# Kernel tuning notes

Hardware: AMD Instinct MI355X
Metric: run time of the kernel (lower is better)

The kernel has to match this reference:

```python
import jax, jax.numpy as jnp
import numpy as np
import math
from math import factorial

EPS = 1e-8
N_ATOMS = 20000
K_NEI = 32
N_RBF = 12
RBF_GAMMA = 1.0
DIMS = [(3, 24), (24, 12), (12, 4)]
# (i, f, o) = (input angular order, filter order, output order), from Convolution.C
CG_PATHS = [(0,0,0),(0,1,1),(1,0,1),(1,1,0),(1,1,1),(1,1,2),(0,2,2),(1,2,1),(1,2,2),(2,2,0),(2,2,1),(2,2,2),(2,0,2),(2,1,1),(2,1,2)]


def _su2_cg(j1, m1, j2, m2, j3, m3):
    if m3 != m1 + m2:
        return 0.0
    f = factorial
    vmin = int(max(-j1 + j2 + m3, -j1 + m1, 0))
    vmax = int(min(j2 + j3 + m1, j3 - j1 + j2, j3 + m3))
    c = ((2 * j3 + 1) * f(j3 + j1 - j2) * f(j3 - j1 + j2) * f(j1 + j2 - j3)
         * f(j3 + m3) * f(j3 - m3)
         / (f(j1 + j2 + j3 + 1) * f(j1 - m1) * f(j1 + m1) * f(j2 - m2) * f(j2 + m2))) ** 0.5
    s = 0.0
    for v in range(vmin, vmax + 1):
        s += (-1) ** (v + j2 + m2) * f(j2 + j3 + m1 - v) * f(j1 - m1 + v) / (
            f(v) * f(j3 - j1 + j2 - v) * f(j3 + m3 - v) * f(j1 - j2 - m3 + v))
    return c * s


def _q(l):
    # change of basis real->complex spherical harmonics (e3nn convention)
    q = np.zeros((2 * l + 1, 2 * l + 1), dtype=complex)
    for m in range(-l, 0):
        q[l + m, l + abs(m)] = 1 / np.sqrt(2)
        q[l + m, l - abs(m)] = -1j / np.sqrt(2)
    q[l, l] = 1.0
    for m in range(1, l + 1):
        q[l + m, l + abs(m)] = (-1) ** m / np.sqrt(2)
        q[l + m, l - abs(m)] = 1j * (-1) ** m / np.sqrt(2)
    return (-1j) ** l * q


def _real_cg(i, f, o):
    C = np.zeros((2 * i + 1, 2 * f + 1, 2 * o + 1), dtype=complex)
    for a, m1 in enumerate(range(-i, i + 1)):
        for b, m2 in enumerate(range(-f, f + 1)):
            for c, m3 in enumerate(range(-o, o + 1)):
                C[a, b, c] = _su2_cg(i, m1, f, m2, o, m3)
    C = np.einsum('ij,kl,mn,ikn->jlm', _q(i), _q(f), np.conj(_q(o).T), C)
    return np.real(C).transpose(2, 0, 1).astype(np.float32)  # [2o+1, 2i+1, 2f+1]


CG = {(i, f, o): jnp.asarray(_real_cg(i, f, o)) for (i, f, o) in CG_PATHS}
RBF_MU = jnp.asarray(np.linspace(0.0, 8.0, N_RBF).astype(np.float32))


def _sh(vec):
    # real spherical harmonics as in class Y (l=1 is the raw vector, l=2 divided by r^2)
    x, y, z = vec[..., 0], vec[..., 1], vec[..., 2]
    r2 = jnp.maximum(x * x + y * y + z * z, EPS)
    y2 = jnp.stack([x * y / r2,
                    y * z / r2,
                    (-x * x - y * y + 2.0 * z * z) / (2.0 * math.sqrt(3.0) * r2),
                    z * x / r2,
                    (x * x - y * y) / (2.0 * r2)], axis=-1)
    return {0: jnp.ones(vec.shape[:-1] + (1,), vec.dtype), 1: vec, 2: y2}


def _ssp(x):  # eta: shifted softplus (SchNet-style scalar nonlinearity)
    return jax.nn.softplus(x) - math.log(2.0)


def _self_interaction(V, w, b):
    O = {k: jnp.einsum('ncm,dc->ndm', Vk, w) for k, Vk in V.items()}
    O[0] = O[0] + b[None, :, None]  # bias only on angular order 0
    return O


def _model(V, nei_idx, Ys, rbf, siA_w, siA_b, rw1, rb1, rw2, rb2, siB_w, siB_b, nl_b):
    V = _self_interaction(V, siA_w, siA_b)
    N, C = nei_idx.shape[0], rw2.shape[1]
    O = {l: jnp.zeros((N, C, 2 * l + 1), rbf.dtype) for l in range(3)}
    for p, (i, f, o) in enumerate(CG_PATHS):
        # per-path radial MLP: 12 -> 12 (relu) -> C
        h = jax.nn.relu(jnp.einsum('nkb,hb->nkh', rbf, rw1[p]) + rb1[p])
        r = jnp.einsum('nkh,ch->nkc', h, rw2[p]) + rb2[p]              # [N,K,C]
        Vg = V[i][nei_idx]                                              # [N,K,C,2i+1]
        cif = jnp.einsum('nkc,nkf,nkci->ncif', r, Ys[f], Vg)            # sum over neighbors
        O[o] = O[o] + jnp.einsum('oif,ncif->nco', CG[(i, f, o)], cif)
    # Norm: per-atom L2 norm over (channel, m)
    V = {k: Vk / jnp.sqrt(jnp.maximum(jnp.sum(Vk * Vk, axis=(1, 2), keepdims=True), EPS))
         for k, Vk in O.items()}
    V = _self_interaction(V, siB_w, siB_b)
    # NonLinearity (faithful to source: norm is taken over ALL atoms and m, per channel)
    out = {0: _ssp(V[0])}
    for k in (1, 2):
        temp = jnp.sqrt(jnp.einsum('acm,acm->c', V[k], V[k])) + nl_b[k - 1]
        out[k] = V[k] * temp[None, :, None]
    return out


def _forward(atom_types, nei_idx, nei_vec, layers, dense):
    N = atom_types.shape[0]
    dt = nei_vec.dtype
    V = {0: jax.nn.one_hot(atom_types, 3, dtype=dt)[:, :, None],
         1: jnp.zeros((N, 3, 3), dt),
         2: jnp.zeros((N, 3, 5), dt)}
    dist = jnp.sqrt(jnp.maximum(jnp.sum(nei_vec * nei_vec, axis=-1), EPS))   # [N,K]
    rbf = jnp.exp(-RBF_GAMMA * (dist[..., None] - RBF_MU) ** 2)              # [N,K,12]
    Ys = _sh(nei_vec)
    for lp in layers:
        V = _model(V, nei_idx, Ys, rbf, *lp)
    E = jnp.sum(V[0], axis=0)[:, 0]                                          # [4]
    dw1, db1, dw2, db2, dw3, db3 = dense
    E = jax.nn.elu(dw1 @ E + db1)
    E = dw2 @ E + db2
    E = dw3 @ E + db3
    return E  # [1]


def setup_inputs() -> dict:
    key = jax.random.key(0)
    ks = iter(jax.random.split(key, 64))
    inp = {}
    inp['atom_types'] = jax.random.randint(next(ks), (N_ATOMS,), 0, 3, dtype=jnp.int32)
    inp['nei_idx'] = jax.random.randint(next(ks), (N_ATOMS, K_NEI), 0, N_ATOMS, dtype=jnp.int32)
    inp['nei_vec'] = jax.random.normal(next(ks), (N_ATOMS, K_NEI, 3), jnp.float32) * 2.0
    for l, (din, dout) in enumerate(DIMS, start=1):
        inp[f'l{l}_siA_w'] = jax.random.normal(next(ks), (dout, din)) / np.sqrt(din)
        inp[f'l{l}_siA_b'] = jnp.zeros((dout,))
        inp[f'l{l}_rw1'] = jax.random.normal(next(ks), (15, N_RBF, N_RBF)) / np.sqrt(N_RBF)
        inp[f'l{l}_rb1'] = jnp.zeros((15, N_RBF))
        inp[f'l{l}_rw2'] = jax.random.normal(next(ks), (15, dout, N_RBF)) / np.sqrt(N_RBF)
        inp[f'l{l}_rb2'] = jnp.zeros((15, dout))
        inp[f'l{l}_siB_w'] = jax.random.normal(next(ks), (dout, dout)) / np.sqrt(dout)
        inp[f'l{l}_siB_b'] = jnp.zeros((dout,))
        inp[f'l{l}_nl_b'] = jnp.zeros((2, dout))
    inp['dense_w1'] = jax.random.normal(next(ks), (4, 4)) * 0.5
    inp['dense_b1'] = jnp.zeros((4,))
    inp['dense_w2'] = jax.random.normal(next(ks), (256, 4)) * 0.5
    inp['dense_b2'] = jnp.zeros((256,))
    inp['dense_w3'] = jax.random.normal(next(ks), (1, 256)) / 16.0
    inp['dense_b3'] = jnp.zeros((1,))
    return inp


def reference(atom_types, nei_idx, nei_vec,
              l1_siA_w, l1_siA_b, l1_rw1, l1_rb1, l1_rw2, l1_rb2, l1_siB_w, l1_siB_b, l1_nl_b,
              l2_siA_w, l2_siA_b, l2_rw1, l2_rb1, l2_rw2, l2_rb2, l2_siB_w, l2_siB_b, l2_nl_b,
              l3_siA_w, l3_siA_b, l3_rw1, l3_rb1, l3_rw2, l3_rb2, l3_siB_w, l3_siB_b, l3_nl_b,
              dense_w1, dense_b1, dense_w2, dense_b2, dense_w3, dense_b3):
    layers = [
        (l1_siA_w, l1_siA_b, l1_rw1, l1_rb1, l1_rw2, l1_rb2, l1_siB_w, l1_siB_b, l1_nl_b),
        (l2_siA_w, l2_siA_b, l2_rw1, l2_rb1, l2_rw2, l2_rb2, l2_siB_w, l2_siB_b, l2_nl_b),
        (l3_siA_w, l3_siA_b, l3_rw1, l3_rb1, l3_rw2, l3_rb2, l3_siB_w, l3_siB_b, l3_nl_b),
    ]
    dense = (dense_w1, dense_b1, dense_w2, dense_b2, dense_w3, dense_b3)
    return _forward(atom_types, nei_idx, nei_vec, layers, dense)
```

## Files before the change

### kernel.cpp

```cpp
#include <hip/hip_runtime.h>
#include <math.h>

typedef long long i64;

#define EPSF 1e-8f

constexpr int NPATH = 15;
constexpr int PI_[NPATH] = {0,0,1,1,1,1,0,1,1,2,2,2,2,2,2};
constexpr int PF_[NPATH] = {0,1,0,1,1,1,2,2,2,2,2,2,0,1,1};
constexpr int PO_[NPATH] = {0,1,1,0,1,2,2,1,2,0,1,2,2,1,2};
constexpr int ISZ[NPATH] = {1,1,3,3,3,3,1,3,3,5,5,5,5,5,5};
constexpr int FSZ[NPATH] = {1,3,1,3,3,3,5,5,5,5,5,5,1,3,3};
constexpr int OSZ[NPATH] = {1,3,3,1,3,5,5,3,5,1,3,5,5,3,5};
constexpr int IBASE[NPATH] = {0,0,1,1,1,1,0,1,1,4,4,4,4,4,4};
constexpr int FBASE[NPATH] = {0,1,0,1,1,1,4,4,4,4,4,4,0,1,1};
constexpr int OBASE[NPATH] = {0,1,1,0,1,4,4,1,4,0,1,4,4,1,4};
constexpr int CGOFF[NPATH+1] = {0,1,10,19,28,55,100,125,170,245,270,345,470,495,540,615};
constexpr int GPOFF[NPATH+1] = {0,4,8,20,24,36,52,60,72,88,96,112,140,168,184,212};
constexpr int CGTOT = 615;
constexpr int GPTOT = 212;

__device__ double dfact(int n){ double r=1.0; for(int i=2;i<=n;++i) r*=(double)i; return r; }

__device__ double su2cg(int j1,int m1,int j2,int m2,int j3,int m3){
  if (m1+m2 != m3) return 0.0;
  int vmin = max(max(-j1+j2+m3, -j1+m1), 0);
  int vmax = min(min(j2+j3+m1, j3-j1+j2), j3+m3);
  if (vmax < vmin) return 0.0;
  double c = sqrt((double)(2*j3+1) * dfact(j3+j1-j2)*dfact(j3-j1+j2)*dfact(j1+j2-j3)
                  * dfact(j3+m3)*dfact(j3-m3)
                  / (dfact(j1+j2+j3+1)*dfact(j1-m1)*dfact(j1+m1)*dfact(j2-m2)*dfact(j2+m2)));
  double s = 0.0;
  for (int v=vmin; v<=vmax; ++v){
    double t = dfact(j2+j3+m1-v)*dfact(j1-m1+v)
             / (dfact(v)*dfact(j3-j1+j2-v)*dfact(j3+m3-v)*dfact(j1-j2-m3+v));
    s += ((v+j2+m2)&1) ? -t : t;
  }
  return c*s;
}

__device__ void qmat_lds(int l, double* qr, double* qi){
  for (int e=0;e<25;e++){ qr[e]=0.0; qi[e]=0.0; }
  const double s2 = 0.70710678118654752440;
  for (int m=-l; m<0; ++m){
    qr[(l+m)*5 + (l-m)] = s2;
    qi[(l+m)*5 + (l+m)] = -s2;
  }
  qr[l*5+l] = 1.0;
  for (int m=1; m<=l; ++m){
    double sg = (m&1)? -1.0 : 1.0;
    qr[(l+m)*5 + (l+m)] = sg*s2;
    qi[(l+m)*5 + (l-m)] = sg*s2;
  }
  if (l==1){
    for (int e=0;e<25;e++){ double r=qr[e], m=qi[e]; qr[e]=m; qi[e]=-r; }
  } else if (l==2){
    for (int e=0;e<25;e++){ qr[e]=-qr[e]; qi[e]=-qi[e]; }
  }
}

__global__ void cg_init_kernel(float* __restrict__ cg){
  int p = blockIdx.x;
  int li = PI_[p], lf = PF_[p], lo = PO_[p];
  int isz = 2*li+1, fsz = 2*lf+1, osz = 2*lo+1;
  __shared__ double sC[125];
  __shared__ double qir[25],qii[25],qfr[25],qfi[25],qor[25],qoi[25];
  if (threadIdx.x==0){
    qmat_lds(li,qir,qii); qmat_lds(lf,qfr,qfi); qmat_lds(lo,qor,qoi);
  }
  int tot = isz*fsz*osz;
  for (int e=threadIdx.x; e<tot; e+=blockDim.x){
    int a = e/(fsz*osz); int r = e%(fsz*osz); int b = r/osz; int n = r%osz;
    sC[e] = su2cg(li, a-li, lf, b-lf, lo, n-lo);
  }
  __syncthreads();
  for (int e=threadIdx.x; e<tot; e+=blockDim.x){
    int mo = e/(isz*fsz); int r = e%(isz*fsz); int ji = r/fsz; int lff = r%fsz;
    double acc = 0.0;
    for (int a=0;a<isz;a++) for(int b=0;b<fsz;b++) for(int n=0;n<osz;n++){
      double s = sC[(a*fsz+b)*osz+n];
      if (s==0.0) continue;
      double r1=qir[a*5+ji],  m1=qii[a*5+ji];
      double r2=qfr[b*5+lff], m2=qfi[b*5+lff];
      double r3=qor[n*5+mo],  m3=-qoi[n*5+mo];
      double rr = r1*r2 - m1*m2;
      double mm = r1*m2 + m1*r2;
      acc += (rr*r3 - mm*m3)*s;
    }
    cg[CGOFF[p] + (mo*isz+ji)*fsz + lff] = (float)acc;
  }
}

__device__ __forceinline__ float sspf(float x){
  float sp = (x > 20.f) ? x : log1pf(__expf(x));
  return sp - 0.69314718055994531f;
}

__global__ void siA1_kernel(const int* __restrict__ types, const float* __restrict__ w,
                            const float* __restrict__ b, float* __restrict__ Vp, int N){
  int idx = blockIdx.x*blockDim.x + threadIdx.x;
  if (idx >= N*24) return;
  int n = idx/24, d = idx%24;
  float v = w[d*3 + types[n]] + b[d];
  float* row = Vp + (i64)idx*12;
  row[0] = v;
  #pragma unroll
  for (int m=1;m<12;m++) row[m]=0.f;
}


template<int A, int P>
__device__ __forceinline__ void gphase(int t, const float* __restrict__ sY,
                                       const float* __restrict__ sCG, float* __restrict__ sG){
  if constexpr (P < NPATH){
    constexpr int gsz = OSZ[P]*ISZ[P];
    for (int e=t; e<gsz*A; e+=192){
      int a = e % A, rel = e / A;
      const float* cr = &sCG[CGOFF[P] + rel*FSZ[P]];
      const float* Yr = &sY[a*12 + FBASE[P]];
      float v = 0.f;
      #pragma unroll
      for (int f=0; f<FSZ[P]; ++f) v += cr[f]*Yr[f];
      sG[a*GPTOT + GPOFF[P] + rel] = v;
    }
    gphase<A,P+1>(t,sY,sCG,sG);
  }
}

template<int P, int V>
__device__ __forceinline__ void gstream(const float* __restrict__ sG_a,
                                        const float* vgr, float* acc){
  constexpr int gsz = OSZ[P]*ISZ[P];
  if constexpr (4*V < gsz){
    float4 g = *reinterpret_cast<const float4*>(&sG_a[GPOFF[P] + 4*V]);
    constexpr int e0 = 4*V;
    acc[OBASE[P] + (e0  )/ISZ[P]] += g.x * vgr[(e0  )%ISZ[P]];
    if constexpr (e0+1 < gsz) acc[OBASE[P] + (e0+1)/ISZ[P]] += g.y * vgr[(e0+1)%ISZ[P]];
    if constexpr (e0+2 < gsz) acc[OBASE[P] + (e0+2)/ISZ[P]] += g.z * vgr[(e0+2)%ISZ[P]];
    if constexpr (e0+3 < gsz) acc[OBASE[P] + (e0+3)/ISZ[P]] += g.w * vgr[(e0+3)%ISZ[P]];
    gstream<P,V+1>(sG_a,vgr,acc);
  }
}

template<int C, int P, int PEND>
__device__ __forceinline__ void ipath(const float* __restrict__ sw2, const float* __restrict__ sb2,
                                      int c, const float* __restrict__ sh_a,
                                      const float* __restrict__ sG_a,
                                      const float* vg, float* acc){
  if constexpr (P < PEND){
    const float* w = &sw2[(P*C+c)*12];
    const float* h = &sh_a[P*12];
    float4 w0 = *reinterpret_cast<const float4*>(w);
    float4 w1 = *reinterpret_cast<const float4*>(w+4);
    float4 w2v= *reinterpret_cast<const float4*>(w+8);
    float4 h0 = *reinterpret_cast<const float4*>(h);
    float4 h1 = *reinterpret_cast<const float4*>(h+4);
    float4 h2 = *reinterpret_cast<const float4*>(h+8);
    float rr = sb2[P*C+c]
      + w0.x*h0.x + w0.y*h0.y + w0.z*h0.z + w0.w*h0.w
      + w1.x*h1.x + w1.y*h1.y + w1.z*h1.z + w1.w*h1.w
      + w2v.x*h2.x + w2v.y*h2.y + w2v.z*h2.z + w2v.w*h2.w;
    float vgr[5];
    #pragma unroll
    for (int i=0; i<ISZ[P]; ++i) vgr[i] = rr * vg[IBASE[P]+i];
    gstream<P,0>(sG_a, vgr, acc);
    ipath<C,P+1,PEND>(sw2,sb2,c,sh_a,sG_a,vg,acc);
  }
}

template<int C, int A, int PG>
__global__ __launch_bounds__(192) void conv_kernel(
    const float* __restrict__ Vp, const int* __restrict__ nei_idx, const float* __restrict__ nei_vec,
    const float* __restrict__ gw1, const float* __restrict__ gb1,
    const float* __restrict__ gw2, const float* __restrict__ gb2,
    const float* __restrict__ cg, float* __restrict__ O, int N)
{
  constexpr int T = 192;
  constexpr int PSPLIT = 10;
  static_assert(PG*A*C == T, "bad geometry");
  __shared__ float sw1[2160];
  __shared__ float sb1[180];
  __shared__ float sw2[15*C*12];
  __shared__ float sb2[15*C];
  __shared__ float sCG[CGTOT];
  __shared__ float srbf[A*12];
  __shared__ float sY[A*12];
  __shared__ float sh[A*180];
  __shared__ float sG[A*GPTOT];

  const int t = threadIdx.x;
  const i64 atom0 = (i64)blockIdx.x * A;

  for (int e=t; e<2160;    e+=T) sw1[e]=gw1[e];
  for (int e=t; e<180;     e+=T) sb1[e]=gb1[e];
  for (int e=t; e<15*C*12; e+=T) sw2[e]=gw2[e];
  for (int e=t; e<15*C;    e+=T) sb2[e]=gb2[e];
  for (int e=t; e<CGTOT;   e+=T) sCG[e]=cg[e];

  auto stage = [&](int k){
    if (t < A){
      i64 at = atom0 + t; if (at >= (i64)N) at = N-1;
      const float* vv = nei_vec + (at*32 + k)*3;
      float x=vv[0], y=vv[1], z=vv[2];
      float r2 = fmaxf(x*x+y*y+z*z, EPSF);
      float d = sqrtf(r2), inv = 1.f/r2;
      float* Re = &srbf[t*12];
      #pragma unroll
      for (int j=0;j<12;++j){ float dd = d - 0.72727272727272727f*(float)j; Re[j] = __expf(-dd*dd); }
      float* Ye = &sY[t*12];
      Ye[0]=1.f; Ye[1]=x; Ye[2]=y; Ye[3]=z;
      Ye[4]=x*y*inv; Ye[5]=y*z*inv;
      Ye[6]=(2.f*z*z - x*x - y*y)*(0.28867513459481287f*inv);
      Ye[7]=z*x*inv; Ye[8]=(x*x - y*y)*(0.5f*inv);
    }
  };

  stage(0);
  __syncthreads();

  const int pg = (PG==2) ? (t/(A*C)) : 0;
  const int rem = (PG==2) ? (t%(A*C)) : t;
  const int a = rem / C;
  const int c = rem % C;

  float acc[9];
  #pragma unroll
  for (int m=0;m<9;++m) acc[m]=0.f;

  for (int k=0; k<32; ++k){
    if (t < 180){
      int p = t/12, hd = t%12;
      const float* w = &sw1[(p*12+hd)*12];
      float4 a0 = *reinterpret_cast<const float4*>(w);
      float4 a1 = *reinterpret_cast<const float4*>(w+4);
      float4 a2 = *reinterpret_cast<const float4*>(w+8);
      float bb = sb1[p*12+hd];
      for (int aa=0; aa<A; ++aa){
        const float* rb = &srbf[aa*12];
        float4 r0 = *reinterpret_cast<const float4*>(rb);
        float4 r1 = *reinterpret_cast<const float4*>(rb+4);
        float4 r2 = *reinterpret_cast<const float4*>(rb+8);
        float v = bb
          + a0.x*r0.x + a0.y*r0.y + a0.z*r0.z + a0.w*r0.w
          + a1.x*r1.x + a1.y*r1.y + a1.z*r1.z + a1.w*r1.w
          + a2.x*r2.x + a2.y*r2.y + a2.z*r2.z + a2.w*r2.w;
        sh[aa*180 + p*12 + hd] = fmaxf(v, 0.f);
      }
    }
    gphase<A,0>(t, sY, sCG, sG);
    __syncthreads();
    if (k+1 < 32) stage(k+1);
    {
      i64 at = atom0 + a; if (at >= (i64)N) at = N-1;
      int nei = nei_idx[at*32 + k];
      const float* vr = Vp + ((i64)nei*C + c)*12;
      float vg[9];
      float4 v0 = *reinterpret_cast<const float4*>(vr);
      float4 v1 = *reinterpret_cast<const float4*>(vr+4);
      vg[0]=v0.x; vg[1]=v0.y; vg[2]=v0.z; vg[3]=v0.w;
      vg[4]=v1.x; vg[5]=v1.y; vg[6]=v1.z; vg[7]=v1.w;
      vg[8]=vr[8];
      if constexpr (PG==1){
        ipath<C,0,NPATH>(sw2,sb2,c,&sh[a*180],&sG[a*GPTOT],vg,acc);
      } else {
        if (pg==0) ipath<C,0,PSPLIT>(sw2,sb2,c,&sh[a*180],&sG[a*GPTOT],vg,acc);
        else       ipath<C,PSPLIT,NPATH>(sw2,sb2,c,&sh[a*180],&sG[a*GPTOT],vg,acc);
      }
    }
    __syncthreads();
  }

  i64 at = atom0 + a;
  if constexpr (PG==1){
    if (at < (i64)N){
      float* orow = O + (at*C + c)*12;
      *reinterpret_cast<float4*>(orow)   = make_float4(acc[0],acc[1],acc[2],acc[3]);
      *reinterpret_cast<float4*>(orow+4) = make_float4(acc[4],acc[5],acc[6],acc[7]);
      orow[8] = acc[8];
    }
  } else {
    if (pg==1){
      float* red = &sh[(a*C+c)*9];
      #pragma unroll
      for (int m=0;m<9;++m) red[m]=acc[m];
    }
    __syncthreads();
    if (pg==0 && at < (i64)N){
      const float* red = &sh[(a*C+c)*9];
      float* orow = O + (at*C + c)*12;
      #pragma unroll
      for (int m=0;m<9;++m) orow[m] = acc[m] + red[m];
    }
  }
}

template<int C>
__global__ __launch_bounds__(64) void normsiB_kernel(
    const float* __restrict__ O, const float* __restrict__ w, const float* __restrict__ b,
    float* __restrict__ Vb, float* __restrict__ gsum, int N)
{
  __shared__ float sW[C*C];
  __shared__ float sO[C*9];
  __shared__ float sg[2*C];
  const int t = threadIdx.x;
  for (int e=t; e<C*C; e+=64) sW[e]=w[e];
  for (int e=t; e<2*C; e+=64) sg[e]=0.f;
  __syncthreads();
  const int iters = (N + gridDim.x - 1)/gridDim.x;
  for (int it=0; it<iters; ++it){
    i64 at = (i64)blockIdx.x + (i64)it*gridDim.x;
    float p0=0.f,p1=0.f,p2=0.f;
    if (at<(i64)N){
      for (int e=t; e<C*9; e+=64){
        int cc=e/9, m=e-cc*9;
        float v = O[((i64)at*C+cc)*12+m];
        sO[e]=v;
        float vv=v*v;
        if (m==0) p0+=vv; else if (m<4) p1+=vv; else p2+=vv;
      }
    }
    #pragma unroll
    for (int off=1; off<64; off<<=1){
      p0 += __shfl_xor(p0, off);
      p1 += __shfl_xor(p1, off);
      p2 += __shfl_xor(p2, off);
    }
    float i0 = 1.f/sqrtf(fmaxf(p0, EPSF));
    float i1 = 1.f/sqrtf(fmaxf(p1, EPSF));
    float i2 = 1.f/sqrtf(fmaxf(p2, EPSF));
    __syncthreads();
    if (at<(i64)N){
      for (int e=t; e<C*9; e+=64){
        int d=e/9, m=e-d*9;
        float inv = (m==0)? i0 : (m<4)? i1 : i2;
        const float* wr = &sW[d*C];
        float s=0.f;
        #pragma unroll
        for (int cc=0; cc<C; ++cc) s += wr[cc]*sO[cc*9+m];
        float outv = s*inv + ((m==0)? b[d] : 0.f);
        Vb[((i64)at*C+d)*12+m]=outv;
        if (m>=1) atomicAdd(&sg[(m<4?0:1)*C + d], outv*outv);
      }
    }
    __syncthreads();
  }
  for (int e=t; e<2*C; e+=64) atomicAdd(&gsum[e], sg[e]);
}

template<int Ci, int Co>
__global__ __launch_bounds__(64) void siaNL_kernel(
    const float* __restrict__ Vb, const float* __restrict__ gsum, const float* __restrict__ nlb,
    const float* __restrict__ w, const float* __restrict__ b, float* __restrict__ Vp, int N)
{
  __shared__ float sW[Co*Ci];
  __shared__ float sIn[Ci*9];
  __shared__ float sT[2*Ci];
  const int t=threadIdx.x;
  for (int e=t; e<Co*Ci; e+=64) sW[e]=w[e];
  for (int e=t; e<2*Ci;  e+=64) sT[e] = sqrtf(gsum[e]) + nlb[e];
  __syncthreads();
  const int iters = (N + gridDim.x - 1)/gridDim.x;
  for (int it=0; it<iters; ++it){
    i64 at = (i64)blockIdx.x + (i64)it*gridDim.x;
    if (at<(i64)N){
      for (int e=t; e<Ci*9; e+=64){
        int cc=e/9, m=e-cc*9;
        float v = Vb[((i64)at*Ci+cc)*12+m];
        float x = (m==0)? sspf(v) : (m<4)? v*sT[cc] : v*sT[Ci+cc];
        sIn[e]=x;
      }
    }
    __syncthreads();
    if (at<(i64)N){
      for (int e=t; e<Co*9; e+=64){
        int d=e/9, m=e-d*9;
        const float* wr=&sW[d*Ci];
        float s = (m==0)? b[d] : 0.f;
        #pragma unroll
        for (int cc=0;cc<Ci;++cc) s += wr[cc]*sIn[cc*9+m];
        Vp[((i64)at*Co+d)*12+m]=s;
      }
    }
    __syncthreads();
  }
}

__global__ void final_reduce_kernel(const float* __restrict__ Vb, float* __restrict__ Eacc, int N){
  __shared__ float sE[4];
  const int t=threadIdx.x;
  if (t<4) sE[t]=0.f;
  __syncthreads();
  float a0=0.f,a1=0.f,a2=0.f,a3=0.f;
  for (i64 at = (i64)blockIdx.x*blockDim.x + t; at < (i64)N; at += (i64)gridDim.x*blockDim.x){
    const float* row = Vb + at*4*12;
    a0 += sspf(row[0]);  a1 += sspf(row[12]);
    a2 += sspf(row[24]); a3 += sspf(row[36]);
  }
  atomicAdd(&sE[0],a0); atomicAdd(&sE[1],a1);
  atomicAdd(&sE[2],a2); atomicAdd(&sE[3],a3);
  __syncthreads();
  if (t<4) atomicAdd(&Eacc[t], sE[t]);
}

__global__ void final_dense_kernel(const float* __restrict__ Eacc,
    const float* __restrict__ w1,const float* __restrict__ b1,
    const float* __restrict__ w2,const float* __restrict__ b2,
    const float* __restrict__ w3,const float* __restrict__ b3,
    float* __restrict__ out)
{
  __shared__ float sE1[4];
  __shared__ float sH[256];
  const int t=threadIdx.x;
  if (t<4){
    float v=b1[t];
    #pragma unroll
    for (int j=0;j<4;j++) v += w1[t*4+j]*Eacc[j];
    sE1[t] = (v>0.f)? v : expm1f(v);
  }
  __syncthreads();
  {
    float v=b2[t];
    #pragma unroll
    for (int j=0;j<4;j++) v += w2[t*4+j]*sE1[j];
    sH[t]=v;
  }
  __syncthreads();
  if (t==0){
    float s=b3[0];
    for (int j=0;j<256;j++) s += w3[j]*sH[j];
    out[0]=s;
  }
}

extern "C" void kernel_launch(void* const* d_in, const int* in_sizes, int n_in,
                              void* d_out, int out_size, void* d_ws, size_t ws_size,
                              hipStream_t stream)
{
  const int* atom_types = (const int*)d_in[0];
  const int* nei_idx    = (const int*)d_in[1];
  const float* nei_vec  = (const float*)d_in[2];
  const float* in_f[36];
  for (int i=0;i<36 && i<n_in;i++) in_f[i] = (const float*)d_in[i];
  const int N = in_sizes[0];

  const i64 bsz = (i64)N*24*12;
  const size_t needed = 8192 + (size_t)3*bsz*4;
  if (ws_size < needed) return;

  char* ws = (char*)d_ws;
  float* cg   = (float*)ws;
  float* accs = (float*)(ws + 4096);
  float* gs1 = accs; float* gs2 = accs+48; float* gs3 = accs+72; float* Eacc = accs+80;
  float* bufA = (float*)(ws + 8192);
  float* bufB = bufA + bsz;
  float* bufC = bufB + bsz;

  #define LP(l, j) in_f[3 + 9*(l) + (j)]
  hipMemsetAsync(accs, 0, 512, stream);
  cg_init_kernel<<<15, 64, 0, stream>>>(cg);

  siA1_kernel<<<(N*24+255)/256, 256, 0, stream>>>(atom_types, LP(0,0), LP(0,1), bufB, N);
  conv_kernel<24,8,1><<<(N+7)/8, 192, 0, stream>>>(bufB, nei_idx, nei_vec,
      LP(0,2),LP(0,3),LP(0,4),LP(0,5), cg, bufC, N);
  normsiB_kernel<24><<<2048,64,0,stream>>>(bufC, LP(0,6), LP(0,7), bufA, gs1, N);
  siaNL_kernel<24,12><<<2048,64,0,stream>>>(bufA, gs1, LP(0,8), LP(1,0), LP(1,1), bufB, N);
  conv_kernel<12,16,1><<<(N+15)/16, 192, 0, stream>>>(bufB, nei_idx, nei_vec,
      LP(1,2),LP(1,3),LP(1,4),LP(1,5), cg, bufC, N);
  normsiB_kernel<12><<<2048,64,0,stream>>>(bufC, LP(1,6), LP(1,7), bufA, gs2, N);
  siaNL_kernel<12,4><<<2048,64,0,stream>>>(bufA, gs2, LP(1,8), LP(2,0), LP(2,1), bufB, N);
  conv_kernel<4,24,2><<<(N+23)/24, 192, 0, stream>>>(bufB, nei_idx, nei_vec,
      LP(2,2),LP(2,3),LP(2,4),LP(2,5), cg, bufC, N);
  normsiB_kernel<4><<<2048,64,0,stream>>>(bufC, LP(2,6), LP(2,7), bufA, gs3, N);
  final_reduce_kernel<<<128,256,0,stream>>>(bufA, Eacc, N);
  final_dense_kernel<<<1,256,0,stream>>>(Eacc, in_f[30],in_f[31],in_f[32],in_f[33],in_f[34],in_f[35],
                                         (float*)d_out);
  #undef LP
}
```

Measured before the change: 2.341 ms.

## Read radial weights from global memory, parallelize RBF staging, split layer-3 paths four ways

Drops the shared-memory copies of the radial MLP weights (w1, w2). Each thread now reads them straight from global memory through cache, which shrinks LDS use per block and removes the per-block weight load. The RBF expansion is spread over A*12 threads instead of A threads. Layer 3 now runs 12 atoms per block with the 15 CG paths split into four groups, reduced through shared memory with vectorized stores. The cost is more global or L1 weight traffic inside the k loop, and a larger shared-memory reduction in layer 3.

```diff
diff --git a/kernel.cpp b/kernel.cpp
--- a/kernel.cpp
+++ b/kernel.cpp
@@ -143,12 +143,12 @@
 }
 
 template<int C, int P, int PEND>
-__device__ __forceinline__ void ipath(const float* __restrict__ sw2, const float* __restrict__ sb2,
+__device__ __forceinline__ void ipath(const float* __restrict__ gw2, const float* __restrict__ sb2,
                                       int c, const float* __restrict__ sh_a,
                                       const float* __restrict__ sG_a,
                                       const float* vg, float* acc){
   if constexpr (P < PEND){
-    const float* w = &sw2[(P*C+c)*12];
+    const float* w = &gw2[(P*C+c)*12];
     const float* h = &sh_a[P*12];
     float4 w0 = *reinterpret_cast<const float4*>(w);
     float4 w1 = *reinterpret_cast<const float4*>(w+4);
@@ -164,7 +164,7 @@
     #pragma unroll
     for (int i=0; i<ISZ[P]; ++i) vgr[i] = rr * vg[IBASE[P]+i];
     gstream<P,0>(sG_a, vgr, acc);
-    ipath<C,P+1,PEND>(sw2,sb2,c,sh_a,sG_a,vg,acc);
+    ipath<C,P+1,PEND>(gw2,sb2,c,sh_a,sG_a,vg,acc);
   }
 }
 
@@ -176,11 +176,8 @@
     const float* __restrict__ cg, float* __restrict__ O, int N)
 {
   constexpr int T = 192;
-  constexpr int PSPLIT = 10;
   static_assert(PG*A*C == T, "bad geometry");
-  __shared__ float sw1[2160];
   __shared__ float sb1[180];
-  __shared__ float sw2[15*C*12];
   __shared__ float sb2[15*C];
   __shared__ float sCG[CGTOT];
   __shared__ float srbf[A*12];
@@ -191,22 +188,26 @@
   const int t = threadIdx.x;
   const i64 atom0 = (i64)blockIdx.x * A;
 
-  for (int e=t; e<2160;    e+=T) sw1[e]=gw1[e];
-  for (int e=t; e<180;     e+=T) sb1[e]=gb1[e];
-  for (int e=t; e<15*C*12; e+=T) sw2[e]=gw2[e];
-  for (int e=t; e<15*C;    e+=T) sb2[e]=gb2[e];
-  for (int e=t; e<CGTOT;   e+=T) sCG[e]=cg[e];
+  for (int e=t; e<180;   e+=T) sb1[e]=gb1[e];
+  for (int e=t; e<15*C;  e+=T) sb2[e]=gb2[e];
+  for (int e=t; e<CGTOT; e+=T) sCG[e]=cg[e];
 
   auto stage = [&](int k){
+    if (t < A*12){
+      int aa = t/12, j = t - aa*12;
+      i64 at = atom0 + aa; if (at >= (i64)N) at = N-1;
+      const float* vv = nei_vec + (at*32 + k)*3;
+      float x=vv[0], y=vv[1], z=vv[2];
+      float d = sqrtf(fmaxf(x*x+y*y+z*z, EPSF));
+      float dd = d - 0.72727272727272727f*(float)j;
+      srbf[aa*12+j] = __expf(-dd*dd);
+    }
     if (t < A){
       i64 at = atom0 + t; if (at >= (i64)N) at = N-1;
       const float* vv = nei_vec + (at*32 + k)*3;
       float x=vv[0], y=vv[1], z=vv[2];
       float r2 = fmaxf(x*x+y*y+z*z, EPSF);
-      float d = sqrtf(r2), inv = 1.f/r2;
-      float* Re = &srbf[t*12];
-      #pragma unroll
-      for (int j=0;j<12;++j){ float dd = d - 0.72727272727272727f*(float)j; Re[j] = __expf(-dd*dd); }
+      float inv = 1.f/r2;
       float* Ye = &sY[t*12];
       Ye[0]=1.f; Ye[1]=x; Ye[2]=y; Ye[3]=z;
       Ye[4]=x*y*inv; Ye[5]=y*z*inv;
@@ -218,8 +219,8 @@
   stage(0);
   __syncthreads();
 
-  const int pg = (PG==2) ? (t/(A*C)) : 0;
-  const int rem = (PG==2) ? (t%(A*C)) : t;
+  const int pg  = (PG==1) ? 0 : (t/(A*C));
+  const int rem = (PG==1) ? t : (t%(A*C));
   const int a = rem / C;
   const int c = rem % C;
 
@@ -229,12 +230,11 @@
 
   for (int k=0; k<32; ++k){
     if (t < 180){
-      int p = t/12, hd = t%12;
-      const float* w = &sw1[(p*12+hd)*12];
+      const float* w = &gw1[t*12];
       float4 a0 = *reinterpret_cast<const float4*>(w);
       float4 a1 = *reinterpret_cast<const float4*>(w+4);
       float4 a2 = *reinterpret_cast<const float4*>(w+8);
-      float bb = sb1[p*12+hd];
+      float bb = sb1[t];
       for (int aa=0; aa<A; ++aa){
         const float* rb = &srbf[aa*12];
         float4 r0 = *reinterpret_cast<const float4*>(rb);
@@ -244,7 +244,7 @@
           + a0.x*r0.x + a0.y*r0.y + a0.z*r0.z + a0.w*r0.w
           + a1.x*r1.x + a1.y*r1.y + a1.z*r1.z + a1.w*r1.w
           + a2.x*r2.x + a2.y*r2.y + a2.z*r2.z + a2.w*r2.w;
-        sh[aa*180 + p*12 + hd] = fmaxf(v, 0.f);
+        sh[aa*180 + t] = fmaxf(v, 0.f);
       }
     }
     gphase<A,0>(t, sY, sCG, sG);
@@ -261,10 +261,15 @@
       vg[4]=v1.x; vg[5]=v1.y; vg[6]=v1.z; vg[7]=v1.w;
       vg[8]=vr[8];
       if constexpr (PG==1){
-        ipath<C,0,NPATH>(sw2,sb2,c,&sh[a*180],&sG[a*GPTOT],vg,acc);
+        ipath<C,0,NPATH>(gw2,sb2,c,&sh[a*180],&sG[a*GPTOT],vg,acc);
+      } else if constexpr (PG==2){
+        if (pg==0) ipath<C,0,10>(gw2,sb2,c,&sh[a*180],&sG[a*GPTOT],vg,acc);
+        else       ipath<C,10,NPATH>(gw2,sb2,c,&sh[a*180],&sG[a*GPTOT],vg,acc);
       } else {
-        if (pg==0) ipath<C,0,PSPLIT>(sw2,sb2,c,&sh[a*180],&sG[a*GPTOT],vg,acc);
-        else       ipath<C,PSPLIT,NPATH>(sw2,sb2,c,&sh[a*180],&sG[a*GPTOT],vg,acc);
+        if      (pg==0) ipath<C,0,5>(gw2,sb2,c,&sh[a*180],&sG[a*GPTOT],vg,acc);
+        else if (pg==1) ipath<C,5,9>(gw2,sb2,c,&sh[a*180],&sG[a*GPTOT],vg,acc);
+        else if (pg==2) ipath<C,9,12>(gw2,sb2,c,&sh[a*180],&sG[a*GPTOT],vg,acc);
+        else            ipath<C,12,NPATH>(gw2,sb2,c,&sh[a*180],&sG[a*GPTOT],vg,acc);
       }
     }
     __syncthreads();
@@ -279,17 +284,23 @@
       orow[8] = acc[8];
     }
   } else {
-    if (pg==1){
-      float* red = &sh[(a*C+c)*9];
+    if (pg > 0){
+      float* red = &sh[((pg-1)*A*C + a*C + c)*9];
       #pragma unroll
       for (int m=0;m<9;++m) red[m]=acc[m];
     }
     __syncthreads();
     if (pg==0 && at < (i64)N){
-      const float* red = &sh[(a*C+c)*9];
+      #pragma unroll
+      for (int g=1; g<PG; ++g){
+        const float* red = &sh[((g-1)*A*C + a*C + c)*9];
+        #pragma unroll
+        for (int m=0;m<9;++m) acc[m] += red[m];
+      }
       float* orow = O + (at*C + c)*12;
-      #pragma unroll
-      for (int m=0;m<9;++m) orow[m] = acc[m] + red[m];
+      *reinterpret_cast<float4*>(orow)   = make_float4(acc[0],acc[1],acc[2],acc[3]);
+      *reinterpret_cast<float4*>(orow+4) = make_float4(acc[4],acc[5],acc[6],acc[7]);
+      orow[8] = acc[8];
     }
   }
 }
@@ -468,7 +479,7 @@
       LP(1,2),LP(1,3),LP(1,4),LP(1,5), cg, bufC, N);
   normsiB_kernel<12><<<2048,64,0,stream>>>(bufC, LP(1,6), LP(1,7), bufA, gs2, N);
   siaNL_kernel<12,4><<<2048,64,0,stream>>>(bufA, gs2, LP(1,8), LP(2,0), LP(2,1), bufB, N);
-  conv_kernel<4,24,2><<<(N+23)/24, 192, 0, stream>>>(bufB, nei_idx, nei_vec,
+  conv_kernel<4,12,4><<<(N+11)/12, 192, 0, stream>>>(bufB, nei_idx, nei_vec,
       LP(2,2),LP(2,3),LP(2,4),LP(2,5), cg, bufC, N);
   normsiB_kernel<4><<<2048,64,0,stream>>>(bufC, LP(2,6), LP(2,7), bufA, gs3, N);
   final_reduce_kernel<<<128,256,0,stream>>>(bufA, Eacc, N);
```

Measured after the change: 3.149 ms. 1.35x slower.
